# Kernel optimization log

Hardware: AMD Instinct MI355X
Metric: run time of the kernel (lower is better)

Reference implementation:

```python
import jax, jax.numpy as jnp
import numpy as np
import math

B, S, D_MODEL, H = 4, 256, 2048, 256
HEAD_DIM = D_MODEL // H  # 8


def setup_inputs() -> dict:
    key = jax.random.key(0)
    ks = jax.random.split(key, 10)
    w_scale = 0.02
    inp = {
        "x": jax.random.normal(ks[0], (B, S, D_MODEL), dtype=jnp.float32),
        "phase_shift": jax.random.normal(ks[1], (H, 1, 1), dtype=jnp.float32),
        "Wq": jax.random.normal(ks[2], (D_MODEL, D_MODEL), dtype=jnp.float32) * w_scale,
        "bq": jnp.zeros((D_MODEL,), dtype=jnp.float32),
        "Wk": jax.random.normal(ks[3], (D_MODEL, D_MODEL), dtype=jnp.float32) * w_scale,
        "bk": jnp.zeros((D_MODEL,), dtype=jnp.float32),
        "Wv": jax.random.normal(ks[4], (D_MODEL, D_MODEL), dtype=jnp.float32) * w_scale,
        "bv": jnp.zeros((D_MODEL,), dtype=jnp.float32),
        "Wo": jax.random.normal(ks[5], (D_MODEL, D_MODEL), dtype=jnp.float32) * w_scale,
        "bo": jnp.zeros((D_MODEL,), dtype=jnp.float32),
    }
    return inp


def _forward(x, phase_shift, Wq, bq, Wk, bk, Wv, bv, Wo, bo):
    b, s, dm = x.shape
    h = phase_shift.shape[0]
    d = dm // h
    # projections (torch Linear with random weights; stored as [in,out])
    q = (x @ Wq + bq).reshape(b, s, h, d)
    k = (x @ Wk + bk).reshape(b, s, h, d)
    v = (x @ Wv + bv).reshape(b, s, h, d)
    # complex phase rotation: q *= exp(+i phi), k *= exp(-i phi)
    # phase_shift (h,1,1) broadcasts against (b,s,h,d) -> varies along the s dim (requires s==h)
    c = jnp.cos(phase_shift)  # (h,1,1)
    sn = jnp.sin(phase_shift)
    qr, qi = q * c, q * sn          # Re/Im of rotated q
    kr, ki = k * c, -(k * sn)       # Re/Im of rotated k
    scale = 1.0 / math.sqrt(d)
    # per-(b,s) head-mixing scores: [b,s,h,h], complex matmul split into real/imag
    sr = (jnp.einsum('bshd,bsgd->bshg', qr, kr)
          - jnp.einsum('bshd,bsgd->bshg', qi, ki)) * scale
    si = (jnp.einsum('bshd,bsgd->bshg', qr, ki)
          + jnp.einsum('bshd,bsgd->bshg', qi, kr)) * scale  # analytically 0 (phases cancel)
    attn_r = jax.nn.softmax(sr, axis=-1)
    attn_i = jax.nn.softmax(si, axis=-1)  # faithful dual softmax; v is real so only
    # Re(attention @ v) = attn_r @ v reaches the output (.real is taken before o_proj)
    del attn_i
    out = jnp.einsum('bshg,bsgd->bshd', attn_r, v).reshape(b, s, dm)
    return out @ Wo + bo


def reference(x, phase_shift, Wq, bq, Wk, bk, Wv, bv, Wo, bo):
    return _forward(x, phase_shift, Wq, bq, Wk, bk, Wv, bv, Wo, bo)
```

## Files before the change

kernel.cpp:

```cpp
#include <hip/hip_runtime.h>
#include <math.h>

#define M_TOK 1024
#define DM    2048
#define NH    256
#define HD    8
#define SCALE 0.35355339059327373f
#define LOG2E 1.4426950408889634f

typedef _Float16 f16x8 __attribute__((ext_vector_type(8)));
typedef _Float16 f16x4 __attribute__((ext_vector_type(4)));
typedef float    f32x4 __attribute__((ext_vector_type(4)));

#if defined(__has_builtin)
#  if __has_builtin(__builtin_amdgcn_exp2f)
#    define EXP2(x) __builtin_amdgcn_exp2f(x)
#  endif
#endif
#ifndef EXP2
#  define EXP2(x) exp2f(x)
#endif

__global__ __launch_bounds__(256) void prep(
    const float* __restrict__ x, _Float16* __restrict__ xh,
    const float* __restrict__ W0, const float* __restrict__ W1,
    const float* __restrict__ W2, const float* __restrict__ W3,
    _Float16* __restrict__ T0, _Float16* __restrict__ T1,
    _Float16* __restrict__ T2, _Float16* __restrict__ T3)
{
    __shared__ float t[64][65];
    const int tid = threadIdx.x;
    const int z   = blockIdx.z;

    if (z == 4) {
        const int i = (blockIdx.y * 32 + blockIdx.x) * 256 + tid;
        const float4 a = ((const float4*)x)[2 * i];
        const float4 b = ((const float4*)x)[2 * i + 1];
        f16x8 v;
        v[0] = (_Float16)a.x; v[1] = (_Float16)a.y; v[2] = (_Float16)a.z; v[3] = (_Float16)a.w;
        v[4] = (_Float16)b.x; v[5] = (_Float16)b.y; v[6] = (_Float16)b.z; v[7] = (_Float16)b.w;
        ((f16x8*)xh)[i] = v;
        return;
    }

    const float* W = (z == 0) ? W0 : (z == 1) ? W1 : (z == 2) ? W2 : W3;
    _Float16*    T = (z == 0) ? T0 : (z == 1) ? T1 : (z == 2) ? T2 : T3;

    const int nb = blockIdx.x * 64;
    const int kb = blockIdx.y * 64;
    const int tr = tid >> 4;
    const int tc = (tid & 15) << 2;

    #pragma unroll
    for (int rr = 0; rr < 4; ++rr) {
        const int k = kb + rr * 16 + tr;
        const float4 v = *(const float4*)&W[(size_t)k * DM + nb + tc];
        t[rr * 16 + tr][tc + 0] = v.x;
        t[rr * 16 + tr][tc + 1] = v.y;
        t[rr * 16 + tr][tc + 2] = v.z;
        t[rr * 16 + tr][tc + 3] = v.w;
    }
    __syncthreads();
    #pragma unroll
    for (int rr = 0; rr < 4; ++rr) {
        const int n = nb + rr * 16 + tr;
        f16x4 v;
        #pragma unroll
        for (int j = 0; j < 4; ++j)
            v[j] = (_Float16)t[tc + j][rr * 16 + tr];
        *(f16x4*)&T[(size_t)n * DM + kb + tc] = v;
    }
}

template<int WGR, int WGC, int WTR, int WTC, bool F16OUT, int MINW, int CS>
__global__ __launch_bounds__(256, MINW) void gemm_db(
    const _Float16* __restrict__ A,
    const _Float16* __restrict__ Bt,
    const float* __restrict__ b0, const float* __restrict__ b1,
    const float* __restrict__ b2, void* __restrict__ C)
{
    constexpr int BM  = WGR * WTR * 16;
    constexpr int BN  = WGC * WTC * 16;
    constexpr int NA  = BM / 8;
    constexpr int NB  = BN / 8;
    constexpr int NC  = NA + NB;
    constexpr int CPW = NC / 4;
    static_assert(NC % 4 == 0);
    constexpr int BUF = (BM + BN) * 64;

    __shared__ _Float16 smem[2 * BUF];

    const int bn = blockIdx.x * BN;
    const int bm = blockIdx.y * BM;

    const int tid  = threadIdx.x;
    const int lane = tid & 63;
    const int wv   = tid >> 6;
    const int wr   = (wv / WGC) * (WTR * 16);
    const int wc   = (wv % WGC) * (WTC * 16);
    const int lr   = lane & 15;
    const int lk   = lane >> 4;
    const int rx   = lr & 7;

    const _Float16* gsrc[CPW];
    int             loff[CPW];
    #pragma unroll
    for (int p = 0; p < CPW; ++p) {
        const int c   = wv * CPW + p;
        const int kch = ((lane & 7) ^ (lane >> 3)) << 3;
        if (c < NA) {
            const int rl = c * 8 + (lane >> 3);
            gsrc[p] = A + (size_t)(bm + rl) * DM + kch;
            loff[p] = c * 512 + lane * 8;
        } else {
            const int rl = (c - NA) * 8 + (lane >> 3);
            gsrc[p] = Bt + (size_t)(bn + rl) * DM + kch;
            loff[p] = BM * 64 + (c - NA) * 512 + lane * 8;
        }
    }

    int offA[WTR][2], offB[WTC][2];
    #pragma unroll
    for (int ks = 0; ks < 2; ++ks) {
        const int sw = (((ks << 2) | lk) ^ rx) << 3;
        #pragma unroll
        for (int i = 0; i < WTR; ++i)
            offA[i][ks] = (wr + i * 16 + lr) * 64 + sw;
        #pragma unroll
        for (int j = 0; j < WTC; ++j)
            offB[j][ks] = BM * 64 + (wc + j * 16 + lr) * 64 + sw;
    }

    f32x4 acc[WTR][WTC] = {};

    auto prefetch = [&](int buf) {
        #pragma unroll
        for (int p = 0; p < CPW; ++p) {
            __builtin_amdgcn_global_load_lds(
                (const __attribute__((address_space(1))) void*)gsrc[p],
                (__attribute__((address_space(3))) void*)(smem + buf * BUF + loff[p]),
                16, 0, 0);
            gsrc[p] += 64;
        }
    };

    auto compute = [&](int buf) {
        const _Float16* base = smem + buf * BUF;
        #pragma unroll
        for (int ks = 0; ks < 2; ++ks) {
            f16x8 aF[WTR], bF[WTC];
            #pragma unroll
            for (int i = 0; i < WTR; ++i)
                aF[i] = *(const f16x8*)&base[offA[i][ks]];
            #pragma unroll
            for (int j = 0; j < WTC; ++j)
                bF[j] = *(const f16x8*)&base[offB[j][ks]];
            #pragma unroll
            for (int i = 0; i < WTR; ++i)
                #pragma unroll
                for (int j = 0; j < WTC; ++j)
                    acc[i][j] = __builtin_amdgcn_mfma_f32_16x16x32_f16(aF[i], bF[j], acc[i][j], 0, 0, 0);
        }
    };

    prefetch(0);
    #pragma unroll 1
    for (int it2 = 0; it2 < 16; ++it2) {
        __syncthreads();
        prefetch(1);
        compute(0);
        __syncthreads();
        if (it2 < 15) prefetch(0);
        compute(1);
    }

    #pragma unroll
    for (int i = 0; i < WTR; ++i) {
        #pragma unroll
        for (int j = 0; j < WTC; ++j) {
            const int col = bn + wc + j * 16 + lr;
            float bv;
            if constexpr (CS > DM) {
                const float* bp = (col < 2048) ? b0 : (col < 4096) ? b1 : b2;
                bv = bp[col & 2047];
            } else {
                bv = b0[col];
            }
            #pragma unroll
            for (int r = 0; r < 4; ++r) {
                const int row = bm + wr + i * 16 + lk * 4 + r;
                const float v = acc[i][j][r] + bv;
                if (F16OUT)
                    ((_Float16*)C)[(size_t)row * CS + col] = (_Float16)v;
                else
                    ((float*)C)[(size_t)row * CS + col] = v;
            }
        }
    }
}

__global__ __launch_bounds__(256) void attn_mfma(
    const _Float16* __restrict__ QKV, _Float16* __restrict__ Oh)
{
    __shared__ _Float16 Vt[8][264];
    __shared__ _Float16 Al[256][72];
    __shared__ _Float16 Ot[256][8];

    const int t    = blockIdx.x;
    const int tid  = threadIdx.x;
    const int lane = tid & 63;
    const int wv   = tid >> 6;
    const int col  = lane & 15;
    const int quad = lane >> 4;
    const int hbase = wv * 64;

    const _Float16* qb = QKV + (size_t)t * (3 * DM);
    const _Float16* kb = qb + DM;
    const _Float16* vb = qb + 2 * DM;

    {
        const f16x8 v = *(const f16x8*)(vb + tid * 8);
        #pragma unroll
        for (int d = 0; d < 8; ++d) Vt[d][tid] = v[d];
    }

    f16x8 qf[4];
    #pragma unroll
    for (int ht = 0; ht < 4; ++ht) {
        f16x8 v = {};
        if (quad == 0)
            v = *(const f16x8*)(qb + (hbase + ht * 16 + col) * 8);
        #pragma unroll
        for (int j = 0; j < 8; ++j) qf[ht][j] = v[j] * (_Float16)(SCALE * LOG2E);
    }

    __syncthreads();

    const f32x4 zf = {};
    float rsum[4] = {};
    f32x4 oacc[4] = {};

    #pragma unroll 1
    for (int c = 0; c < 4; ++c) {
        const int gchunk = c * 64;

        f16x8 kf[4];
        #pragma unroll
        for (int gt = 0; gt < 4; ++gt) {
            f16x8 v = {};
            if (quad == 0)
                v = *(const f16x8*)(kb + (gchunk + gt * 16 + col) * 8);
            kf[gt] = v;
        }

        f32x4 s[4][4];
        #pragma unroll
        for (int gt = 0; gt < 4; ++gt)
            #pragma unroll
            for (int ht = 0; ht < 4; ++ht)
                s[gt][ht] = __builtin_amdgcn_mfma_f32_16x16x32_f16(kf[gt], qf[ht], zf, 0, 0, 0);

        #pragma unroll
        for (int gt = 0; gt < 4; ++gt) {
            #pragma unroll
            for (int ht = 0; ht < 4; ++ht) {
                f16x4 e4;
                #pragma unroll
                for (int r = 0; r < 4; ++r) {
                    e4[r] = (_Float16)EXP2(s[gt][ht][r]);
                    rsum[ht] += (float)e4[r];
                }
                *(f16x4*)&Al[hbase + ht * 16 + col][gt * 16 + quad * 4] = e4;
            }
        }

        #pragma unroll
        for (int ks = 0; ks < 2; ++ks) {
            f16x8 vf = {};
            if (col < 8)
                vf = *(const f16x8*)&Vt[col][gchunk + ks * 32 + quad * 8];
            #pragma unroll
            for (int ht = 0; ht < 4; ++ht) {
                const f16x8 af = *(const f16x8*)&Al[hbase + ht * 16 + col][ks * 32 + quad * 8];
                oacc[ht] = __builtin_amdgcn_mfma_f32_16x16x32_f16(af, vf, oacc[ht], 0, 0, 0);
            }
        }
    }

    #pragma unroll
    for (int ht = 0; ht < 4; ++ht) {
        rsum[ht] += __shfl_xor(rsum[ht], 16, 64);
        rsum[ht] += __shfl_xor(rsum[ht], 32, 64);
    }

    #pragma unroll
    for (int ht = 0; ht < 4; ++ht) {
        #pragma unroll
        for (int r = 0; r < 4; ++r) {
            const float sh = __shfl(rsum[ht], quad * 4 + r, 64);
            const float v  = oacc[ht][r] / sh;
            if (col < 8)
                Ot[hbase + ht * 16 + quad * 4 + r][col] = (_Float16)v;
        }
    }
    const f16x8 ov = *(const f16x8*)&Ot[tid][0];
    *(f16x8*)(Oh + (size_t)t * DM + tid * 8) = ov;
}

extern "C" void kernel_launch(void* const* d_in, const int* in_sizes, int n_in,
                              void* d_out, int out_size, void* d_ws, size_t ws_size,
                              hipStream_t stream)
{
    const float* x  = (const float*)d_in[0];
    const float* Wq = (const float*)d_in[2];
    const float* bq = (const float*)d_in[3];
    const float* Wk = (const float*)d_in[4];
    const float* bk = (const float*)d_in[5];
    const float* Wv = (const float*)d_in[6];
    const float* bv = (const float*)d_in[7];
    const float* Wo = (const float*)d_in[8];
    const float* bo = (const float*)d_in[9];
    float* out = (float*)d_out;

    char* ws = (char*)d_ws;
    _Float16* xh  = (_Float16*)(ws);
    _Float16* Wt  = (_Float16*)(ws + (4u  << 20));
    _Float16* Wto = (_Float16*)(ws + (28u << 20));
    _Float16* QKV = (_Float16*)(ws + (36u << 20));
    _Float16* Oh  = (_Float16*)(ws + (48u << 20));

    prep<<<dim3(32, 32, 5), dim3(256), 0, stream>>>(
        x, xh, Wq, Wk, Wv, Wo,
        Wt, Wt + 2048 * 2048, Wt + 2 * 2048 * 2048, Wto);

    gemm_db<2, 2, 4, 3, true, 2, 3 * DM><<<dim3(64, 8), dim3(256), 0, stream>>>(
        xh, Wt, bq, bk, bv, (void*)QKV);

    attn_mfma<<<dim3(M_TOK), dim3(256), 0, stream>>>(QKV, Oh);

    gemm_db<1, 4, 2, 2, false, 3, DM><<<dim3(16, 32), dim3(256), 0, stream>>>(
        Oh, Wto, bo, bo, bo, (void*)out);
}
```

Measured before the change: 196.8 us.

## Deepen GEMM prefetch pipeline with explicit vmcnt waits and process two tokens per attention block

Result: faster. 191.7 us (-2.6%).

```diff
diff --git a/kernel.cpp b/kernel.cpp
--- a/kernel.cpp
+++ b/kernel.cpp
@@ -20,6 +20,26 @@
 #ifndef EXP2
 #  define EXP2(x) exp2f(x)
 #endif
+
+template<int N>
+__device__ __forceinline__ void vm_wait() {
+    if constexpr (N == 0) asm volatile("s_waitcnt vmcnt(0)" ::: "memory");
+    else if constexpr (N == 1) asm volatile("s_waitcnt vmcnt(1)" ::: "memory");
+    else if constexpr (N == 2) asm volatile("s_waitcnt vmcnt(2)" ::: "memory");
+    else if constexpr (N == 3) asm volatile("s_waitcnt vmcnt(3)" ::: "memory");
+    else if constexpr (N == 4) asm volatile("s_waitcnt vmcnt(4)" ::: "memory");
+    else if constexpr (N == 5) asm volatile("s_waitcnt vmcnt(5)" ::: "memory");
+    else if constexpr (N == 6) asm volatile("s_waitcnt vmcnt(6)" ::: "memory");
+    else if constexpr (N == 7) asm volatile("s_waitcnt vmcnt(7)" ::: "memory");
+    else if constexpr (N == 8) asm volatile("s_waitcnt vmcnt(8)" ::: "memory");
+    else static_assert(N <= 8, "add vmcnt case");
+}
+
+__device__ __forceinline__ void raw_barrier() {
+    asm volatile("" ::: "memory");
+    __builtin_amdgcn_s_barrier();
+    asm volatile("" ::: "memory");
+}
 
 __global__ __launch_bounds__(256) void prep(
     const float* __restrict__ x, _Float16* __restrict__ xh,
@@ -155,23 +175,26 @@
             #pragma unroll
             for (int j = 0; j < WTC; ++j)
                 bF[j] = *(const f16x8*)&base[offB[j][ks]];
+            __builtin_amdgcn_s_setprio(1);
             #pragma unroll
             for (int i = 0; i < WTR; ++i)
                 #pragma unroll
                 for (int j = 0; j < WTC; ++j)
                     acc[i][j] = __builtin_amdgcn_mfma_f32_16x16x32_f16(aF[i], bF[j], acc[i][j], 0, 0, 0);
+            __builtin_amdgcn_s_setprio(0);
         }
     };
 
     prefetch(0);
+    prefetch(1);
     #pragma unroll 1
-    for (int it2 = 0; it2 < 16; ++it2) {
-        __syncthreads();
-        prefetch(1);
-        compute(0);
-        __syncthreads();
-        if (it2 < 15) prefetch(0);
-        compute(1);
+    for (int t = 0; t < 32; ++t) {
+        if (t < 31) vm_wait<CPW>();
+        else        vm_wait<0>();
+        raw_barrier();
+        compute(t & 1);
+        raw_barrier();
+        if (t < 30) prefetch(t & 1);
     }
 
     #pragma unroll
@@ -206,7 +229,6 @@
     __shared__ _Float16 Al[256][72];
     __shared__ _Float16 Ot[256][8];
 
-    const int t    = blockIdx.x;
     const int tid  = threadIdx.x;
     const int lane = tid & 63;
     const int wv   = tid >> 6;
@@ -214,97 +236,103 @@
     const int quad = lane >> 4;
     const int hbase = wv * 64;
 
-    const _Float16* qb = QKV + (size_t)t * (3 * DM);
-    const _Float16* kb = qb + DM;
-    const _Float16* vb = qb + 2 * DM;
-
-    {
-        const f16x8 v = *(const f16x8*)(vb + tid * 8);
-        #pragma unroll
-        for (int d = 0; d < 8; ++d) Vt[d][tid] = v[d];
-    }
-
-    f16x8 qf[4];
-    #pragma unroll
-    for (int ht = 0; ht < 4; ++ht) {
-        f16x8 v = {};
-        if (quad == 0)
-            v = *(const f16x8*)(qb + (hbase + ht * 16 + col) * 8);
-        #pragma unroll
-        for (int j = 0; j < 8; ++j) qf[ht][j] = v[j] * (_Float16)(SCALE * LOG2E);
-    }
-
-    __syncthreads();
-
-    const f32x4 zf = {};
-    float rsum[4] = {};
-    f32x4 oacc[4] = {};
-
     #pragma unroll 1
-    for (int c = 0; c < 4; ++c) {
-        const int gchunk = c * 64;
-
-        f16x8 kf[4];
-        #pragma unroll
-        for (int gt = 0; gt < 4; ++gt) {
+    for (int tt = 0; tt < 2; ++tt) {
+        const int t = blockIdx.x * 2 + tt;
+        const _Float16* qb = QKV + (size_t)t * (3 * DM);
+        const _Float16* kb = qb + DM;
+        const _Float16* vb = qb + 2 * DM;
+
+        __syncthreads();
+
+        {
+            const f16x8 v = *(const f16x8*)(vb + tid * 8);
+            #pragma unroll
+            for (int d = 0; d < 8; ++d) Vt[d][tid] = v[d];
+        }
+
+        f16x8 qf[4];
+        #pragma unroll
+        for (int ht = 0; ht < 4; ++ht) {
             f16x8 v = {};
             if (quad == 0)
-                v = *(const f16x8*)(kb + (gchunk + gt * 16 + col) * 8);
-            kf[gt] = v;
-        }
-
-        f32x4 s[4][4];
-        #pragma unroll
-        for (int gt = 0; gt < 4; ++gt)
-            #pragma unroll
-            for (int ht = 0; ht < 4; ++ht)
-                s[gt][ht] = __builtin_amdgcn_mfma_f32_16x16x32_f16(kf[gt], qf[ht], zf, 0, 0, 0);
-
-        #pragma unroll
-        for (int gt = 0; gt < 4; ++gt) {
-            #pragma unroll
-            for (int ht = 0; ht < 4; ++ht) {
-                f16x4 e4;
+                v = *(const f16x8*)(qb + (hbase + ht * 16 + col) * 8);
+            #pragma unroll
+            for (int j = 0; j < 8; ++j) qf[ht][j] = v[j] * (_Float16)(SCALE * LOG2E);
+        }
+
+        __syncthreads();
+
+        const f32x4 zf = {};
+        float rsum[4] = {};
+        f32x4 oacc[4] = {};
+
+        #pragma unroll 1
+        for (int c = 0; c < 4; ++c) {
+            const int gchunk = c * 64;
+
+            f16x8 kf[4];
+            #pragma unroll
+            for (int gt = 0; gt < 4; ++gt) {
+                f16x8 v = {};
+                if (quad == 0)
+                    v = *(const f16x8*)(kb + (gchunk + gt * 16 + col) * 8);
+                kf[gt] = v;
+            }
+
+            f32x4 s[4][4];
+            #pragma unroll
+            for (int gt = 0; gt < 4; ++gt)
                 #pragma unroll
-                for (int r = 0; r < 4; ++r) {
-                    e4[r] = (_Float16)EXP2(s[gt][ht][r]);
-                    rsum[ht] += (float)e4[r];
+                for (int ht = 0; ht < 4; ++ht)
+                    s[gt][ht] = __builtin_amdgcn_mfma_f32_16x16x32_f16(kf[gt], qf[ht], zf, 0, 0, 0);
+
+            #pragma unroll
+            for (int gt = 0; gt < 4; ++gt) {
+                #pragma unroll
+                for (int ht = 0; ht < 4; ++ht) {
+                    f16x4 e4;
+                    #pragma unroll
+                    for (int r = 0; r < 4; ++r) {
+                        e4[r] = (_Float16)EXP2(s[gt][ht][r]);
+                        rsum[ht] += (float)e4[r];
+                    }
+                    *(f16x4*)&Al[hbase + ht * 16 + col][gt * 16 + quad * 4] = e4;
                 }
-                *(f16x4*)&Al[hbase + ht * 16 + col][gt * 16 + quad * 4] = e4;
-            }
-        }
-
-        #pragma unroll
-        for (int ks = 0; ks < 2; ++ks) {
-            f16x8 vf = {};
-            if (col < 8)
-                vf = *(const f16x8*)&Vt[col][gchunk + ks * 32 + quad * 8];
-            #pragma unroll
-            for (int ht = 0; ht < 4; ++ht) {
-                const f16x8 af = *(const f16x8*)&Al[hbase + ht * 16 + col][ks * 32 + quad * 8];
-                oacc[ht] = __builtin_amdgcn_mfma_f32_16x16x32_f16(af, vf, oacc[ht], 0, 0, 0);
-            }
-        }
-    }
-
-    #pragma unroll
-    for (int ht = 0; ht < 4; ++ht) {
-        rsum[ht] += __shfl_xor(rsum[ht], 16, 64);
-        rsum[ht] += __shfl_xor(rsum[ht], 32, 64);
-    }
-
-    #pragma unroll
-    for (int ht = 0; ht < 4; ++ht) {
-        #pragma unroll
-        for (int r = 0; r < 4; ++r) {
-            const float sh = __shfl(rsum[ht], quad * 4 + r, 64);
-            const float v  = oacc[ht][r] / sh;
-            if (col < 8)
-                Ot[hbase + ht * 16 + quad * 4 + r][col] = (_Float16)v;
-        }
-    }
-    const f16x8 ov = *(const f16x8*)&Ot[tid][0];
-    *(f16x8*)(Oh + (size_t)t * DM + tid * 8) = ov;
+            }
+
+            #pragma unroll
+            for (int ks = 0; ks < 2; ++ks) {
+                f16x8 vf = {};
+                if (col < 8)
+                    vf = *(const f16x8*)&Vt[col][gchunk + ks * 32 + quad * 8];
+                #pragma unroll
+                for (int ht = 0; ht < 4; ++ht) {
+                    const f16x8 af = *(const f16x8*)&Al[hbase + ht * 16 + col][ks * 32 + quad * 8];
+                    oacc[ht] = __builtin_amdgcn_mfma_f32_16x16x32_f16(af, vf, oacc[ht], 0, 0, 0);
+                }
+            }
+        }
+
+        #pragma unroll
+        for (int ht = 0; ht < 4; ++ht) {
+            rsum[ht] += __shfl_xor(rsum[ht], 16, 64);
+            rsum[ht] += __shfl_xor(rsum[ht], 32, 64);
+        }
+
+        #pragma unroll
+        for (int ht = 0; ht < 4; ++ht) {
+            #pragma unroll
+            for (int r = 0; r < 4; ++r) {
+                const float sh = __shfl(rsum[ht], quad * 4 + r, 64);
+                const float v  = oacc[ht][r] / sh;
+                if (col < 8)
+                    Ot[hbase + ht * 16 + quad * 4 + r][col] = (_Float16)v;
+            }
+        }
+        const f16x8 ov = *(const f16x8*)&Ot[tid][0];
+        *(f16x8*)(Oh + (size_t)t * DM + tid * 8) = ov;
+    }
 }
 
 extern "C" void kernel_launch(void* const* d_in, const int* in_sizes, int n_in,
@@ -336,7 +364,7 @@
     gemm_db<2, 2, 4, 3, true, 2, 3 * DM><<<dim3(64, 8), dim3(256), 0, stream>>>(
         xh, Wt, bq, bk, bv, (void*)QKV);
 
-    attn_mfma<<<dim3(M_TOK), dim3(256), 0, stream>>>(QKV, Oh);
+    attn_mfma<<<dim3(M_TOK / 2), dim3(256), 0, stream>>>(QKV, Oh);
 
     gemm_db<1, 4, 2, 2, false, 3, DM><<<dim3(16, 32), dim3(256), 0, stream>>>(
         Oh, Wto, bo, bo, bo, (void*)out);
```
